# Kernel optimization log

Hardware: AMD Instinct MI355X
Metric: run time of the kernel (lower is better)

## Reference

```python
import jax, jax.numpy as jnp
import numpy as np

LN_EPS = 1e-3  # Keras LayerNormalization default epsilon
EPS = 1e-8     # slot-attention weight epsilon
NUM_ITERS = 3


def layer_norm(x, g, b):
    m = jnp.mean(x, axis=-1, keepdims=True)
    v = jnp.var(x, axis=-1, keepdims=True)
    return g * (x - m) * jax.lax.rsqrt(v + LN_EPS) + b


def gru_cell(x, h, Wx, Wh, b_in, b_rec):
    # Keras GRUCell (reset_after=True): separate input and recurrent biases
    gx = x @ Wx + b_in      # [K, 3D]
    gh = h @ Wh + b_rec     # [K, 3D]
    xz, xr, xh = jnp.split(gx, 3, axis=-1)
    hz, hr, hh = jnp.split(gh, 3, axis=-1)
    z = jax.nn.sigmoid(xz + hz)
    r = jax.nn.sigmoid(xr + hr)
    h_cand = jnp.tanh(xh + r * hh)
    return z * h + (1.0 - z) * h_cand


def setup_inputs() -> dict:
    key = jax.random.key(0)
    N, C, D, H, K = 262144, 64, 64, 128, 4
    ks = jax.random.split(key, 32)
    w = lambda k, s: (jax.random.normal(k, s, jnp.float32) * 0.02)
    inp = {
        "x": jax.random.normal(ks[0], (N, C), jnp.float32),
        "noise_fg": jax.random.normal(ks[1], (K - 1, D), jnp.float32),
        "noise_bg": jax.random.normal(ks[2], (1, D), jnp.float32),
        "ln_in_g": jnp.ones((C,), jnp.float32),
        "ln_in_b": jnp.zeros((C,), jnp.float32),
        "mu_fg": w(ks[3], (1, D)),
        "log_sigma_fg": w(ks[4], (1, D)),
        "mu_bg": w(ks[5], (1, D)),
        "log_sigma_bg": w(ks[6], (1, D)),
        "Wk": w(ks[7], (C, D)),
        "Wv": w(ks[8], (C, D)),
        "qfg_g": jnp.ones((D,), jnp.float32),
        "qfg_b": jnp.zeros((D,), jnp.float32),
        "Wq_fg": w(ks[9], (D, D)),
        "qbg_g": jnp.ones((D,), jnp.float32),
        "qbg_b": jnp.zeros((D,), jnp.float32),
        "Wq_bg": w(ks[10], (D, D)),
        "gru_fg_Wx": w(ks[11], (D, 3 * D)),
        "gru_fg_Wh": w(ks[12], (D, 3 * D)),
        "gru_fg_bin": jnp.zeros((3 * D,), jnp.float32),
        "gru_fg_brec": jnp.zeros((3 * D,), jnp.float32),
        "gru_bg_Wx": w(ks[13], (D, 3 * D)),
        "gru_bg_Wh": w(ks[14], (D, 3 * D)),
        "gru_bg_bin": jnp.zeros((3 * D,), jnp.float32),
        "gru_bg_brec": jnp.zeros((3 * D,), jnp.float32),
        "mfg_g": jnp.ones((D,), jnp.float32),
        "mfg_b": jnp.zeros((D,), jnp.float32),
        "mfg_W1": w(ks[15], (D, H)),
        "mfg_b1": jnp.zeros((H,), jnp.float32),
        "mfg_W2": w(ks[16], (H, D)),
        "mfg_b2": jnp.zeros((D,), jnp.float32),
        "mbg_g": jnp.ones((D,), jnp.float32),
        "mbg_b": jnp.zeros((D,), jnp.float32),
        "mbg_W1": w(ks[17], (D, H)),
        "mbg_b1": jnp.zeros((H,), jnp.float32),
        "mbg_W2": w(ks[18], (H, D)),
        "mbg_b2": jnp.zeros((D,), jnp.float32),
    }
    return inp


def reference(x, noise_fg, noise_bg, ln_in_g, ln_in_b, mu_fg, log_sigma_fg, mu_bg,
              log_sigma_bg, Wk, Wv, qfg_g, qfg_b, Wq_fg, qbg_g, qbg_b, Wq_bg,
              gru_fg_Wx, gru_fg_Wh, gru_fg_bin, gru_fg_brec,
              gru_bg_Wx, gru_bg_Wh, gru_bg_bin, gru_bg_brec,
              mfg_g, mfg_b, mfg_W1, mfg_b1, mfg_W2, mfg_b2,
              mbg_g, mbg_b, mbg_W1, mbg_b1, mbg_W2, mbg_b2):
    D = Wk.shape[1]
    scale = D ** (-0.5)
    x = layer_norm(x, ln_in_g, ln_in_b)
    k = x @ Wk  # [N, D]
    v = x @ Wv  # [N, D]
    slots_fg = mu_fg + jnp.exp(log_sigma_fg) * noise_fg  # [K-1, D]
    slots_bg = mu_bg + jnp.exp(log_sigma_bg) * noise_bg  # [1, D]
    attn = None
    for _ in range(NUM_ITERS):
        q_fg = layer_norm(slots_fg, qfg_g, qfg_b) @ Wq_fg * scale  # [K-1, D]
        q_bg = layer_norm(slots_bg, qbg_g, qbg_b) @ Wq_bg * scale  # [1, D]
        logits = jnp.concatenate([k @ q_bg.T, k @ q_fg.T], axis=-1)  # [N, K]
        attn = jax.nn.softmax(logits, axis=-1)  # competition over slots
        w_all = attn + EPS
        w_all = w_all / jnp.sum(w_all, axis=0, keepdims=True)  # normalize over N
        updates = w_all.T @ v  # [K, D]
        upd_bg, upd_fg = updates[:1], updates[1:]
        slots_bg = gru_cell(upd_bg, slots_bg, gru_bg_Wx, gru_bg_Wh, gru_bg_bin, gru_bg_brec)
        slots_fg = gru_cell(upd_fg, slots_fg, gru_fg_Wx, gru_fg_Wh, gru_fg_bin, gru_fg_brec)
        h_bg = jax.nn.relu(layer_norm(slots_bg, mbg_g, mbg_b) @ mbg_W1 + mbg_b1)
        slots_bg = slots_bg + h_bg @ mbg_W2 + mbg_b2
        h_fg = jax.nn.relu(layer_norm(slots_fg, mfg_g, mfg_b) @ mfg_W1 + mfg_b1)
        slots_fg = slots_fg + h_fg @ mfg_W2 + mfg_b2
    slots = jnp.concatenate([slots_bg, slots_fg], axis=0)  # [K, D]
    return slots, attn.T  # attn: [K, N]
```

## Files before the change

kernel.cpp:

```cpp
#include <hip/hip_runtime.h>
#include <hip/hip_bf16.h>

#define N_ROWS   262144
#define TILES    1024
#define LN_EPS_F 1e-3f
#define EPS_W    1e-8f
#define NEPS_F   (262144.0f*1e-8f)

__device__ __forceinline__ float bf2f(unsigned u){ return __uint_as_float((u&0xffffu)<<16); }
__device__ __forceinline__ ushort f2bf(float f){
  unsigned u = __float_as_uint(f);
  return (ushort)((u + 0x7fffu + ((u>>16)&1u)) >> 16);
}
__device__ __forceinline__ unsigned cvtpk(float lo, float hi){
  unsigned r;
  asm("v_cvt_pk_bf16_f32 %0, %1, %2" : "=v"(r) : "v"(lo), "v"(hi));
  return r;
}
__device__ __forceinline__ float wave_sum64(float v){
#pragma unroll
  for (int off=1; off<64; off<<=1) v += __shfl_xor(v, off);
  return v;
}

__global__ __launch_bounds__(256) void attn_pass_kernel(
    const float* __restrict__ x, uint* __restrict__ xhat,
    const float* __restrict__ ucoef, float* __restrict__ pT,
    float* __restrict__ attn_out, int first, int last)
{
  __shared__ __align__(16) ushort xs[64*256];
  __shared__ __align__(16) uint2 attn_s[256];
  __shared__ __align__(16) float qs[256];
  __shared__ float qc[4];
  const int tid = threadIdx.x;
  const int w = tid>>6, ln = tid&63;
  const int lm = ln&15, lg = ln>>4;
  qs[tid] = ucoef[tid];
  if (tid < 4) qc[tid] = ucoef[256+tid];

  const size_t r0 = (size_t)blockIdx.x*256;

  if (first){
#pragma unroll
    for (int mi = 0; mi < 4; ++mi){
      const int trow = w*64 + mi*16 + lm;
      const float* xr = &x[(r0 + trow)*64 + lg*8];
      const float4 a0 = *(const float4*)xr;
      const float4 a1 = *(const float4*)(xr+4);
      const float4 b0 = *(const float4*)(xr+32);
      const float4 b1 = *(const float4*)(xr+36);
      float s1 = ((a0.x+a0.y)+(a0.z+a0.w)) + ((a1.x+a1.y)+(a1.z+a1.w))
               + ((b0.x+b0.y)+(b0.z+b0.w)) + ((b1.x+b1.y)+(b1.z+b1.w));
      float s2 = a0.x*a0.x; s2=fmaf(a0.y,a0.y,s2); s2=fmaf(a0.z,a0.z,s2); s2=fmaf(a0.w,a0.w,s2);
      s2=fmaf(a1.x,a1.x,s2); s2=fmaf(a1.y,a1.y,s2); s2=fmaf(a1.z,a1.z,s2); s2=fmaf(a1.w,a1.w,s2);
      s2=fmaf(b0.x,b0.x,s2); s2=fmaf(b0.y,b0.y,s2); s2=fmaf(b0.z,b0.z,s2); s2=fmaf(b0.w,b0.w,s2);
      s2=fmaf(b1.x,b1.x,s2); s2=fmaf(b1.y,b1.y,s2); s2=fmaf(b1.z,b1.z,s2); s2=fmaf(b1.w,b1.w,s2);
      s1 += __shfl_xor(s1,16); s2 += __shfl_xor(s2,16);
      s1 += __shfl_xor(s1,32); s2 += __shfl_xor(s2,32);
      const float m  = s1*(1.0f/64.0f);
      const float rs = rsqrtf(s2*(1.0f/64.0f) - m*m + LN_EPS_F);
      const float nm = -m*rs;
      float xv[16];
      xv[0]=fmaf(a0.x,rs,nm); xv[1]=fmaf(a0.y,rs,nm); xv[2]=fmaf(a0.z,rs,nm); xv[3]=fmaf(a0.w,rs,nm);
      xv[4]=fmaf(a1.x,rs,nm); xv[5]=fmaf(a1.y,rs,nm); xv[6]=fmaf(a1.z,rs,nm); xv[7]=fmaf(a1.w,rs,nm);
      xv[8]=fmaf(b0.x,rs,nm); xv[9]=fmaf(b0.y,rs,nm); xv[10]=fmaf(b0.z,rs,nm); xv[11]=fmaf(b0.w,rs,nm);
      xv[12]=fmaf(b1.x,rs,nm); xv[13]=fmaf(b1.y,rs,nm); xv[14]=fmaf(b1.z,rs,nm); xv[15]=fmaf(b1.w,rs,nm);
      const int ch = trow>>3, rr2 = trow&7;
#pragma unroll
      for (int p = 0; p < 8; ++p){
        const int d = lg*8 + p;
        xs[d*256 + ((ch ^ ((d*5)&31))<<3) + rr2] = (ushort)cvtpk(xv[p], xv[p]);
      }
#pragma unroll
      for (int p = 0; p < 8; ++p){
        const int d = 32 + lg*8 + p;
        xs[d*256 + ((ch ^ ((d*5)&31))<<3) + rr2] = (ushort)cvtpk(xv[8+p], xv[8+p]);
      }
    }
    __syncthreads();
#pragma unroll
    for (int k = 0; k < 8; ++k){
      const int i = k*256 + tid;
      const uint4 v = *(const uint4*)&xs[i*8];
      *(uint4*)&xhat[(size_t)blockIdx.x*8192 + i*4] = v;
    }
  } else {
#pragma unroll
    for (int k = 0; k < 8; ++k){
      const int i = k*256 + tid;
      const uint4 v = *(const uint4*)&xhat[(size_t)blockIdx.x*8192 + i*4];
      *(uint4*)&xs[i*8] = v;
    }
    __syncthreads();
  }

  const int lrow = w*64 + lm*4;
  float la[4][4];
#pragma unroll
  for (int r = 0; r < 4; ++r)
#pragma unroll
    for (int s = 0; s < 4; ++s) la[r][s] = 0.f;
#pragma unroll
  for (int dd = 0; dd < 16; ++dd){
    const int d = lg*16 + dd;
    const uint2 kk = *(const uint2*)&xs[d*256 + (((lrow>>3) ^ ((d*5)&31))<<3) + (lrow&7)];
    const float e0 = bf2f(kk.x), e1 = bf2f(kk.x>>16);
    const float e2 = bf2f(kk.y), e3 = bf2f(kk.y>>16);
    const float4 q4 = *(const float4*)&qs[d*4];
#pragma unroll
    for (int s = 0; s < 4; ++s){
      const float qv = (s==0)?q4.x:(s==1)?q4.y:(s==2)?q4.z:q4.w;
      la[0][s] = fmaf(e0, qv, la[0][s]);
      la[1][s] = fmaf(e1, qv, la[1][s]);
      la[2][s] = fmaf(e2, qv, la[2][s]);
      la[3][s] = fmaf(e3, qv, la[3][s]);
    }
  }
#pragma unroll
  for (int r = 0; r < 4; ++r)
#pragma unroll
    for (int s = 0; s < 4; ++s){
      la[r][s] += __shfl_xor(la[r][s], 16);
      la[r][s] += __shfl_xor(la[r][s], 32);
      la[r][s] += qc[s];
    }

  float av[4][4];
  float cs0=0.f, cs1=0.f, cs2=0.f, cs3=0.f;
#pragma unroll
  for (int r = 0; r < 4; ++r){
    const float mx = fmaxf(fmaxf(la[r][0],la[r][1]), fmaxf(la[r][2],la[r][3]));
    const float e0 = __expf(la[r][0]-mx), e1 = __expf(la[r][1]-mx);
    const float e2 = __expf(la[r][2]-mx), e3 = __expf(la[r][3]-mx);
    const float inv = 1.0f/((e0+e1)+(e2+e3));
    av[r][0]=e0*inv; av[r][1]=e1*inv; av[r][2]=e2*inv; av[r][3]=e3*inv;
    cs0 += av[r][0]; cs1 += av[r][1]; cs2 += av[r][2]; cs3 += av[r][3];
  }
  if (lg == 0){
#pragma unroll
    for (int r = 0; r < 4; ++r){
      uint2 pk;
      pk.x = cvtpk(av[r][0], av[r][1]);
      pk.y = cvtpk(av[r][2], av[r][3]);
      attn_s[lrow + r] = pk;
    }
    if (last){
#pragma unroll
      for (int s = 0; s < 4; ++s){
        float4 o; o.x=av[0][s]; o.y=av[1][s]; o.z=av[2][s]; o.w=av[3][s];
        *(float4*)&attn_out[(size_t)s*N_ROWS + r0 + lrow] = o;
      }
    }
  }
  cs0 = wave_sum64(cs0)*0.25f; cs1 = wave_sum64(cs1)*0.25f;
  cs2 = wave_sum64(cs2)*0.25f; cs3 = wave_sum64(cs3)*0.25f;

  float n0=0.f,n1=0.f,n2=0.f,n3=0.f, vs=0.f;
#pragma unroll
  for (int rb = 0; rb < 8; ++rb){
    const int ch = w*8 + rb;
    const uint4 vv = *(const uint4*)&xs[ln*256 + ((ch ^ ((ln*5)&31))<<3)];
    const ushort* vp = (const ushort*)&vv;
#pragma unroll
    for (int k2 = 0; k2 < 8; ++k2){
      const uint2 au = attn_s[ch*8 + k2];
      const float b0 = bf2f(au.x), b1 = bf2f(au.x>>16);
      const float b2 = bf2f(au.y), b3 = bf2f(au.y>>16);
      const float vvv = bf2f((unsigned)vp[k2]);
      n0 = fmaf(b0, vvv, n0); n1 = fmaf(b1, vvv, n1);
      n2 = fmaf(b2, vvv, n2); n3 = fmaf(b3, vvv, n3);
      vs += vvv;
    }
  }

  __syncthreads();
  float* fp = (float*)xs;
  fp[w*256 + 0*64 + ln] = n0;
  fp[w*256 + 1*64 + ln] = n1;
  fp[w*256 + 2*64 + ln] = n2;
  fp[w*256 + 3*64 + ln] = n3;
  fp[1024 + w*64 + ln] = vs;
  if (ln == 0){ fp[1280+w*4+0]=cs0; fp[1280+w*4+1]=cs1; fp[1280+w*4+2]=cs2; fp[1280+w*4+3]=cs3; }
  __syncthreads();
  float* pb = pT + (size_t)blockIdx.x*324;
  pb[tid] = fp[tid] + fp[256+tid] + fp[512+tid] + fp[768+tid];
  if (tid < 64)
    pb[256 + tid] = fp[1024+tid] + fp[1088+tid] + fp[1152+tid] + fp[1216+tid];
  if (tid < 4)
    pb[320 + tid] = fp[1280+tid] + fp[1284+tid] + fp[1288+tid] + fp[1292+tid];
}

__global__ __launch_bounds__(512) void update_kernel(int mode,
    const float* __restrict__ pT,
    float* __restrict__ slots, float* __restrict__ ucoef, float* __restrict__ out,
    const float* __restrict__ noise_fg, const float* __restrict__ noise_bg,
    const float* __restrict__ mu_fg, const float* __restrict__ ls_fg,
    const float* __restrict__ mu_bg, const float* __restrict__ ls_bg,
    const float* __restrict__ ln_g, const float* __restrict__ ln_b,
    const float* __restrict__ Wk, const float* __restrict__ Wv,
    const float* __restrict__ qfg_g, const float* __restrict__ qfg_b, const float* __restrict__ Wq_fg,
    const float* __restrict__ qbg_g, const float* __restrict__ qbg_b, const float* __restrict__ Wq_bg,
    const float* __restrict__ gfWx, const float* __restrict__ gfWh,
    const float* __restrict__ gfbin, const float* __restrict__ gfbrec,
    const float* __restrict__ gbWx, const float* __restrict__ gbWh,
    const float* __restrict__ gbbin, const float* __restrict__ gbbrec,
    const float* __restrict__ mfg_g, const float* __restrict__ mfg_b,
    const float* __restrict__ mfW1, const float* __restrict__ mfb1,
    const float* __restrict__ mfW2, const float* __restrict__ mfb2,
    const float* __restrict__ mbg_g, const float* __restrict__ mbg_b,
    const float* __restrict__ mbW1, const float* __restrict__ mbb1,
    const float* __restrict__ mbW2, const float* __restrict__ mbb2)
{
  const int j = blockIdx.x;
  const int tid = threadIdx.x;
  const int ln = tid & 63, wv = tid >> 6;
  const bool bg = (j == 0);

  __shared__ __align__(16) float wlds[24640];
  __shared__ float bi_s[192], br_s[192], b1_s[128], b2_s[64];
  __shared__ float mg_s[64], mbv_s[64], qg_s[64], qb_s[64], gl_s[64], bl_s[64];
  __shared__ float vin_s[64], u_s[64], h_s[64], hg_s[64], l_s[64], h1_s[128], ql_s[64];
  __shared__ float gxp[2][192], ghp[2][192];
  __shared__ float pn_s[8][64], pv_s[8][64], csw[8];
  __shared__ float p4[4][128], p8[8][64];

  const float* __restrict__ Wx = bg?gbWx:gfWx;  const float* __restrict__ Wh = bg?gbWh:gfWh;
  const float* __restrict__ bi = bg?gbbin:gfbin; const float* __restrict__ br = bg?gbbrec:gfbrec;
  const float* __restrict__ W1 = bg?mbW1:mfW1;  const float* __restrict__ b1 = bg?mbb1:mfb1;
  const float* __restrict__ W2 = bg?mbW2:mfW2;  const float* __restrict__ b2 = bg?mbb2:mfb2;
  const float* __restrict__ Wq = bg?Wq_bg:Wq_fg;

  const int WQOFF  = (mode == 0) ? 0 : 16384;
  const int WKTOFF = (mode == 0) ? 4096 : 20480;

  float hnew = 0.f;

  if (mode == 0) {
    { const float4* s = (const float4*)Wq; float4* d = (float4*)wlds;
#pragma unroll
      for (int i = 0; i < 2; ++i) d[tid + i*512] = s[tid + i*512]; }
#pragma unroll
    for (int k = 0; k < 8; ++k){
      const int i = tid + k*512;
      wlds[4096 + (i&63)*65 + (i>>6)] = Wk[i];
    }
    if (tid < 64){
      qg_s[tid] = (bg?qbg_g:qfg_g)[tid]; qb_s[tid] = (bg?qbg_b:qfg_b)[tid];
      gl_s[tid] = ln_g[tid]; bl_s[tid] = ln_b[tid];
      hnew = bg ? fmaf(expf(ls_bg[tid]), noise_bg[tid], mu_bg[tid])
                : fmaf(expf(ls_fg[tid]), noise_fg[(j-1)*64+tid], mu_fg[tid]);
      slots[j*64 + tid] = hnew;
    }
    __syncthreads();
  } else {
    if (tid < 192){ bi_s[tid] = bi[tid]; br_s[tid] = br[tid]; }
    else if (tid < 320){ const int i2 = tid-192; b1_s[i2] = b1[i2]; }
    else if (tid < 384){ const int i2 = tid-320; b2_s[i2] = b2[i2]; }
    else if (tid < 448){ const int i2 = tid-384; mg_s[i2] = (bg?mbg_g:mfg_g)[i2]; mbv_s[i2] = (bg?mbg_b:mfg_b)[i2]; }
    else               { const int i2 = tid-448; qg_s[i2] = (bg?qbg_g:qfg_g)[i2]; qb_s[i2] = (bg?qbg_b:qfg_b)[i2]; }
    if (tid < 64){ gl_s[tid] = ln_g[tid]; bl_s[tid] = ln_b[tid]; }
    { const float4* sA = (const float4*)Wx; const float4* sB = (const float4*)Wh;
      float4* dA = (float4*)wlds; float4* dB = (float4*)(wlds + 12288);
#pragma unroll
      for (int i = 0; i < 6; ++i){ dA[tid + i*512] = sA[tid + i*512]; dB[tid + i*512] = sB[tid + i*512]; } }

    {
      float a0 = 0.f, a1 = 0.f, a2 = 0.f;
      float c0 = 0.f, c1v = 0.f, c2v = 0.f;
      for (int bb = 0; bb < TILES/8; bb += 16){
#pragma unroll
        for (int u = 0; u < 16; u += 2){
          const float* pa = pT + (size_t)((bb+u  )*8 + wv)*324;
          const float* pc = pT + (size_t)((bb+u+1)*8 + wv)*324;
          a0 += pa[j*64 + ln];  a1 += pa[256 + ln];  a2 += pa[320 + j];
          c0 += pc[j*64 + ln];  c1v += pc[256 + ln]; c2v += pc[320 + j];
        }
      }
      pn_s[wv][ln] = a0 + c0; pv_s[wv][ln] = a1 + c1v;
      if (ln == 0) csw[wv] = a2 + c2v;
    }
    if (tid < 64) h_s[tid] = slots[j*64 + tid];
    __syncthreads();
    if (tid < 64) {
      const float csum = ((csw[0]+csw[1])+(csw[2]+csw[3])) + ((csw[4]+csw[5])+(csw[6]+csw[7])) + NEPS_F;
      float nm = 0.f, vm = 0.f;
#pragma unroll
      for (int p2 = 0; p2 < 8; ++p2){ nm += pn_s[p2][tid]; vm += pv_s[p2][tid]; }
      vin_s[tid] = gl_s[tid]*(nm + EPS_W*vm)/csum + bl_s[tid];
    }
    __syncthreads();
    { const int p8i = tid >> 6;
      float a = 0.f;
      float wbuf[8];
#pragma unroll
      for (int dd = 0; dd < 8; ++dd) wbuf[dd] = Wv[(p8i*8+dd)*64 + ln];
#pragma unroll
      for (int dd = 0; dd < 8; ++dd) a = fmaf(vin_s[p8i*8+dd], wbuf[dd], a);
      p8[p8i][ln] = a;
    }
    __syncthreads();
    if (tid < 64)
      u_s[tid] = ((p8[0][tid]+p8[1][tid])+(p8[2][tid]+p8[3][tid]))
               + ((p8[4][tid]+p8[5][tid])+(p8[6][tid]+p8[7][tid]));
    __syncthreads();
    if (tid < 384) {
      const int gcol = tid % 192, gp = tid / 192;
      float ax = 0.f, ah = 0.f;
#pragma unroll
      for (int dd = 0; dd < 32; ++dd) {
        ax = fmaf(u_s[gp*32+dd], wlds[(gp*32+dd)*192 + gcol], ax);
        ah = fmaf(h_s[gp*32+dd], wlds[12288 + (gp*32+dd)*192 + gcol], ah);
      }
      gxp[gp][gcol] = ax; ghp[gp][gcol] = ah;
    }
    __syncthreads();
    { const float4* s1 = (const float4*)W1; const float4* s2 = (const float4*)W2; const float4* s3 = (const float4*)Wq;
      float4* d1 = (float4*)wlds; float4* d2 = (float4*)(wlds + 8192); float4* d3 = (float4*)(wlds + 16384);
#pragma unroll
      for (int i = 0; i < 4; ++i){ d1[tid + i*512] = s1[tid + i*512]; d2[tid + i*512] = s2[tid + i*512]; }
#pragma unroll
      for (int i = 0; i < 2; ++i){ d3[tid + i*512] = s3[tid + i*512]; }
#pragma unroll
      for (int k = 0; k < 8; ++k){
        const int i = tid + k*512;
        wlds[20480 + (i&63)*65 + (i>>6)] = Wk[i];
      } }
    if (tid < 64) {
      const float gx0 = gxp[0][tid]     + gxp[1][tid]     + bi_s[tid];
      const float gh0 = ghp[0][tid]     + ghp[1][tid]     + br_s[tid];
      const float gx1 = gxp[0][64+tid]  + gxp[1][64+tid]  + bi_s[64+tid];
      const float gh1 = ghp[0][64+tid]  + ghp[1][64+tid]  + br_s[64+tid];
      const float gx2 = gxp[0][128+tid] + gxp[1][128+tid] + bi_s[128+tid];
      const float gh2 = ghp[0][128+tid] + ghp[1][128+tid] + br_s[128+tid];
      const float h  = h_s[tid];
      const float z  = 1.f/(1.f + expf(-(gx0 + gh0)));
      const float rr = 1.f/(1.f + expf(-(gx1 + gh1)));
      const float hc = tanhf(gx2 + rr*gh2);
      const float hg = z*h + (1.f - z)*hc;
      hg_s[tid] = hg;
      const float m  = wave_sum64(hg) * (1.f/64.f);
      const float vr = wave_sum64((hg-m)*(hg-m)) * (1.f/64.f);
      const float rs = rsqrtf(vr + LN_EPS_F);
      l_s[tid] = mg_s[tid]*(hg-m)*rs + mbv_s[tid];
    }
    __syncthreads();
    { const int p4i = tid >> 7, hi = tid & 127;
      float a = 0.f;
#pragma unroll
      for (int dd = 0; dd < 16; ++dd) a = fmaf(l_s[p4i*16+dd], wlds[(p4i*16+dd)*128 + hi], a);
      p4[p4i][hi] = a;
    }
    __syncthreads();
    if (tid < 128) h1_s[tid] = fmaxf(((p4[0][tid]+p4[1][tid])+(p4[2][tid]+p4[3][tid])) + b1_s[tid], 0.f);
    __syncthreads();
    { const int p8i = tid >> 6;
      float a = 0.f;
#pragma unroll
      for (int dd = 0; dd < 16; ++dd) a = fmaf(h1_s[p8i*16+dd], wlds[8192 + (p8i*16+dd)*64 + ln], a);
      p8[p8i][ln] = a;
    }
    __syncthreads();
    if (tid < 64) {
      hnew = hg_s[tid] + b2_s[tid]
           + ((p8[0][tid]+p8[1][tid])+(p8[2][tid]+p8[3][tid]))
           + ((p8[4][tid]+p8[5][tid])+(p8[6][tid]+p8[7][tid]));
      slots[j*64 + tid] = hnew;
    }
  }

  if (mode == 3) {
    if (tid < 64) out[j*64 + tid] = hnew;
  } else {
    if (tid < 64) {
      const float m  = wave_sum64(hnew) * (1.f/64.f);
      const float vr = wave_sum64((hnew-m)*(hnew-m)) * (1.f/64.f);
      const float rs = rsqrtf(vr + LN_EPS_F);
      l_s[tid] = qg_s[tid]*(hnew-m)*rs + qb_s[tid];
    }
    __syncthreads();
    { const int p8i = tid >> 6;
      float a = 0.f;
#pragma unroll
      for (int dd = 0; dd < 8; ++dd) a = fmaf(l_s[p8i*8+dd], wlds[WQOFF + (p8i*8+dd)*64 + ln], a);
      p8[p8i][ln] = a;
    }
    __syncthreads();
    if (tid < 64)
      ql_s[tid] = (((p8[0][tid]+p8[1][tid])+(p8[2][tid]+p8[3][tid]))
                  +((p8[4][tid]+p8[5][tid])+(p8[6][tid]+p8[7][tid]))) * 0.125f;
    __syncthreads();
    if (tid < 256){
      const int d = tid & 63, pt = tid >> 6;
      float ts = 0.f;
#pragma unroll
      for (int oo = 0; oo < 16; ++oo){
        const int o = pt*16 + oo;
        ts = fmaf(wlds[WKTOFF + o*65 + d], ql_s[o], ts);
      }
      p8[pt][d] = ts;
    }
    __syncthreads();
    if (tid < 64){
      const float t = (p8[0][tid]+p8[1][tid]) + (p8[2][tid]+p8[3][tid]);
      ucoef[tid*4 + j] = gl_s[tid]*t;
      const float c = wave_sum64(bl_s[tid]*t);
      if (tid == 0) ucoef[256 + j] = c;
    }
  }
}

extern "C" void kernel_launch(void* const* d_in, const int* in_sizes, int n_in,
                              void* d_out, int out_size, void* d_ws, size_t ws_size,
                              hipStream_t stream)
{
  const float* x        = (const float*)d_in[0];
  const float* noise_fg = (const float*)d_in[1];
  const float* noise_bg = (const float*)d_in[2];
  const float* ln_g     = (const float*)d_in[3];
  const float* ln_b     = (const float*)d_in[4];
  const float* mu_fg    = (const float*)d_in[5];
  const float* ls_fg    = (const float*)d_in[6];
  const float* mu_bg    = (const float*)d_in[7];
  const float* ls_bg    = (const float*)d_in[8];
  const float* Wk       = (const float*)d_in[9];
  const float* Wv       = (const float*)d_in[10];
  const float* qfg_g    = (const float*)d_in[11];
  const float* qfg_b    = (const float*)d_in[12];
  const float* Wq_fg    = (const float*)d_in[13];
  const float* qbg_g    = (const float*)d_in[14];
  const float* qbg_b    = (const float*)d_in[15];
  const float* Wq_bg    = (const float*)d_in[16];
  const float* gfWx     = (const float*)d_in[17];
  const float* gfWh     = (const float*)d_in[18];
  const float* gfbin    = (const float*)d_in[19];
  const float* gfbrec   = (const float*)d_in[20];
  const float* gbWx     = (const float*)d_in[21];
  const float* gbWh     = (const float*)d_in[22];
  const float* gbbin    = (const float*)d_in[23];
  const float* gbbrec   = (const float*)d_in[24];
  const float* mfg_g    = (const float*)d_in[25];
  const float* mfg_b    = (const float*)d_in[26];
  const float* mfW1     = (const float*)d_in[27];
  const float* mfb1     = (const float*)d_in[28];
  const float* mfW2     = (const float*)d_in[29];
  const float* mfb2     = (const float*)d_in[30];
  const float* mbg_g    = (const float*)d_in[31];
  const float* mbg_b    = (const float*)d_in[32];
  const float* mbW1     = (const float*)d_in[33];
  const float* mbb1     = (const float*)d_in[34];
  const float* mbW2     = (const float*)d_in[35];
  const float* mbb2     = (const float*)d_in[36];

  float* out = (float*)d_out;

  char* ws = (char*)d_ws;
  uint*  xhat  = (uint*)ws;
  float* fws   = (float*)(ws + (size_t)TILES*8192*4);
  float* slots = fws;
  float* ucoef = fws + 256;
  float* pT    = fws + 1024;

  auto launch_update = [&](int mode){
    update_kernel<<<4, 512, 0, stream>>>(mode, pT, slots, ucoef, out,
      noise_fg, noise_bg, mu_fg, ls_fg, mu_bg, ls_bg, ln_g, ln_b, Wk, Wv,
      qfg_g, qfg_b, Wq_fg, qbg_g, qbg_b, Wq_bg,
      gfWx, gfWh, gfbin, gfbrec, gbWx, gbWh, gbbin, gbbrec,
      mfg_g, mfg_b, mfW1, mfb1, mfW2, mfb2,
      mbg_g, mbg_b, mbW1, mbb1, mbW2, mbb2);
  };

  launch_update(0);
  for (int it = 0; it < 3; ++it) {
    attn_pass_kernel<<<TILES, 256, 0, stream>>>(x, xhat, ucoef, pT, out + 256,
                                                it==0 ? 1 : 0, it==2 ? 1 : 0);
    launch_update(it+1);
  }
}
```

Baseline: 109.7 us.

## Fuse initial slot/query setup into first attention pass and process two tiles per block

Removes the separate mode-0 update launch by having every attention block recompute the initial slots, layer norm, query projection and Wk folding itself, with block 0 writing the slots. The attention kernel now runs 512 blocks that each handle two 256-row chunks, accumulating partials across chunks and prefetching the next chunk's xhat into registers while the current one computes. This halves the partial-sum count the update kernel must reduce and drops one launch. In exchange, every block redoes small redundant matmuls in the first pass and there are fewer blocks to spread across CUs.

```diff
diff --git a/kernel.cpp b/kernel.cpp
--- a/kernel.cpp
+++ b/kernel.cpp
@@ -2,16 +2,13 @@
 #include <hip/hip_bf16.h>
 
 #define N_ROWS   262144
-#define TILES    1024
+#define ATT_BLOCKS 512
+#define CHUNKS   2
 #define LN_EPS_F 1e-3f
 #define EPS_W    1e-8f
 #define NEPS_F   (262144.0f*1e-8f)
 
 __device__ __forceinline__ float bf2f(unsigned u){ return __uint_as_float((u&0xffffu)<<16); }
-__device__ __forceinline__ ushort f2bf(float f){
-  unsigned u = __float_as_uint(f);
-  return (ushort)((u + 0x7fffu + ((u>>16)&1u)) >> 16);
-}
 __device__ __forceinline__ unsigned cvtpk(float lo, float hi){
   unsigned r;
   asm("v_cvt_pk_bf16_f32 %0, %1, %2" : "=v"(r) : "v"(lo), "v"(hi));
@@ -26,154 +23,209 @@
 __global__ __launch_bounds__(256) void attn_pass_kernel(
     const float* __restrict__ x, uint* __restrict__ xhat,
     const float* __restrict__ ucoef, float* __restrict__ pT,
-    float* __restrict__ attn_out, int first, int last)
+    float* __restrict__ attn_out, float* __restrict__ slots,
+    const float* __restrict__ noise_fg, const float* __restrict__ noise_bg,
+    const float* __restrict__ mu_fg, const float* __restrict__ ls_fg,
+    const float* __restrict__ mu_bg, const float* __restrict__ ls_bg,
+    const float* __restrict__ ln_g, const float* __restrict__ ln_b,
+    const float* __restrict__ Wk,
+    const float* __restrict__ qfg_g, const float* __restrict__ qfg_b, const float* __restrict__ Wq_fg,
+    const float* __restrict__ qbg_g, const float* __restrict__ qbg_b, const float* __restrict__ Wq_bg,
+    int first, int last)
 {
   __shared__ __align__(16) ushort xs[64*256];
   __shared__ __align__(16) uint2 attn_s[256];
   __shared__ __align__(16) float qs[256];
   __shared__ float qc[4];
+  __shared__ float l4[256], q4s[256];
   const int tid = threadIdx.x;
   const int w = tid>>6, ln = tid&63;
   const int lm = ln&15, lg = ln>>4;
-  qs[tid] = ucoef[tid];
-  if (tid < 4) qc[tid] = ucoef[256+tid];
-
-  const size_t r0 = (size_t)blockIdx.x*256;
+  const int blk = blockIdx.x;
 
   if (first){
-#pragma unroll
-    for (int mi = 0; mi < 4; ++mi){
-      const int trow = w*64 + mi*16 + lm;
-      const float* xr = &x[(r0 + trow)*64 + lg*8];
-      const float4 a0 = *(const float4*)xr;
-      const float4 a1 = *(const float4*)(xr+4);
-      const float4 b0 = *(const float4*)(xr+32);
-      const float4 b1 = *(const float4*)(xr+36);
-      float s1 = ((a0.x+a0.y)+(a0.z+a0.w)) + ((a1.x+a1.y)+(a1.z+a1.w))
-               + ((b0.x+b0.y)+(b0.z+b0.w)) + ((b1.x+b1.y)+(b1.z+b1.w));
-      float s2 = a0.x*a0.x; s2=fmaf(a0.y,a0.y,s2); s2=fmaf(a0.z,a0.z,s2); s2=fmaf(a0.w,a0.w,s2);
-      s2=fmaf(a1.x,a1.x,s2); s2=fmaf(a1.y,a1.y,s2); s2=fmaf(a1.z,a1.z,s2); s2=fmaf(a1.w,a1.w,s2);
-      s2=fmaf(b0.x,b0.x,s2); s2=fmaf(b0.y,b0.y,s2); s2=fmaf(b0.z,b0.z,s2); s2=fmaf(b0.w,b0.w,s2);
-      s2=fmaf(b1.x,b1.x,s2); s2=fmaf(b1.y,b1.y,s2); s2=fmaf(b1.z,b1.z,s2); s2=fmaf(b1.w,b1.w,s2);
-      s1 += __shfl_xor(s1,16); s2 += __shfl_xor(s2,16);
-      s1 += __shfl_xor(s1,32); s2 += __shfl_xor(s2,32);
-      const float m  = s1*(1.0f/64.0f);
-      const float rs = rsqrtf(s2*(1.0f/64.0f) - m*m + LN_EPS_F);
-      const float nm = -m*rs;
-      float xv[16];
-      xv[0]=fmaf(a0.x,rs,nm); xv[1]=fmaf(a0.y,rs,nm); xv[2]=fmaf(a0.z,rs,nm); xv[3]=fmaf(a0.w,rs,nm);
-      xv[4]=fmaf(a1.x,rs,nm); xv[5]=fmaf(a1.y,rs,nm); xv[6]=fmaf(a1.z,rs,nm); xv[7]=fmaf(a1.w,rs,nm);
-      xv[8]=fmaf(b0.x,rs,nm); xv[9]=fmaf(b0.y,rs,nm); xv[10]=fmaf(b0.z,rs,nm); xv[11]=fmaf(b0.w,rs,nm);
-      xv[12]=fmaf(b1.x,rs,nm); xv[13]=fmaf(b1.y,rs,nm); xv[14]=fmaf(b1.z,rs,nm); xv[15]=fmaf(b1.w,rs,nm);
-      const int ch = trow>>3, rr2 = trow&7;
-#pragma unroll
-      for (int p = 0; p < 8; ++p){
-        const int d = lg*8 + p;
-        xs[d*256 + ((ch ^ ((d*5)&31))<<3) + rr2] = (ushort)cvtpk(xv[p], xv[p]);
-      }
-#pragma unroll
-      for (int p = 0; p < 8; ++p){
-        const int d = 32 + lg*8 + p;
-        xs[d*256 + ((ch ^ ((d*5)&31))<<3) + rr2] = (ushort)cvtpk(xv[8+p], xv[8+p]);
-      }
-    }
+    const float h0 = (w==0) ? fmaf(expf(ls_bg[ln]), noise_bg[ln], mu_bg[ln])
+                            : fmaf(expf(ls_fg[ln]), noise_fg[(w-1)*64+ln], mu_fg[ln]);
+    if (blk == 0) slots[w*64+ln] = h0;
+    const float m  = wave_sum64(h0) * (1.f/64.f);
+    const float vr = wave_sum64((h0-m)*(h0-m)) * (1.f/64.f);
+    const float rs = rsqrtf(vr + LN_EPS_F);
+    l4[tid] = (w==0?qbg_g:qfg_g)[ln]*(h0-m)*rs + (w==0?qbg_b:qfg_b)[ln];
     __syncthreads();
-#pragma unroll
-    for (int k = 0; k < 8; ++k){
-      const int i = k*256 + tid;
-      const uint4 v = *(const uint4*)&xs[i*8];
-      *(uint4*)&xhat[(size_t)blockIdx.x*8192 + i*4] = v;
+    {
+      const float* __restrict__ Wqj = (w==0) ? Wq_bg : Wq_fg;
+      float acc = 0.f;
+#pragma unroll
+      for (int dd = 0; dd < 64; ++dd) acc = fmaf(l4[w*64+dd], Wqj[dd*64+ln], acc);
+      q4s[tid] = acc * 0.125f;
+    }
+    __syncthreads();
+    {
+      float t = 0.f;
+#pragma unroll
+      for (int oo = 0; oo < 64; ++oo) t = fmaf(Wk[ln*64+oo], q4s[w*64+oo], t);
+      qs[ln*4 + w] = ln_g[ln]*t;
+      const float cc = wave_sum64(ln_b[ln]*t);
+      if (ln == 0) qc[w] = cc;
     }
   } else {
-#pragma unroll
-    for (int k = 0; k < 8; ++k){
-      const int i = k*256 + tid;
-      const uint4 v = *(const uint4*)&xhat[(size_t)blockIdx.x*8192 + i*4];
-      *(uint4*)&xs[i*8] = v;
-    }
-    __syncthreads();
-  }
-
-  const int lrow = w*64 + lm*4;
-  float la[4][4];
-#pragma unroll
-  for (int r = 0; r < 4; ++r)
-#pragma unroll
-    for (int s = 0; s < 4; ++s) la[r][s] = 0.f;
-#pragma unroll
-  for (int dd = 0; dd < 16; ++dd){
-    const int d = lg*16 + dd;
-    const uint2 kk = *(const uint2*)&xs[d*256 + (((lrow>>3) ^ ((d*5)&31))<<3) + (lrow&7)];
-    const float e0 = bf2f(kk.x), e1 = bf2f(kk.x>>16);
-    const float e2 = bf2f(kk.y), e3 = bf2f(kk.y>>16);
-    const float4 q4 = *(const float4*)&qs[d*4];
-#pragma unroll
-    for (int s = 0; s < 4; ++s){
-      const float qv = (s==0)?q4.x:(s==1)?q4.y:(s==2)?q4.z:q4.w;
-      la[0][s] = fmaf(e0, qv, la[0][s]);
-      la[1][s] = fmaf(e1, qv, la[1][s]);
-      la[2][s] = fmaf(e2, qv, la[2][s]);
-      la[3][s] = fmaf(e3, qv, la[3][s]);
-    }
-  }
-#pragma unroll
-  for (int r = 0; r < 4; ++r)
-#pragma unroll
-    for (int s = 0; s < 4; ++s){
-      la[r][s] += __shfl_xor(la[r][s], 16);
-      la[r][s] += __shfl_xor(la[r][s], 32);
-      la[r][s] += qc[s];
-    }
-
-  float av[4][4];
+    qs[tid] = ucoef[tid];
+    if (tid < 4) qc[tid] = ucoef[256+tid];
+  }
+  __syncthreads();
+
+  float n0=0.f,n1=0.f,n2=0.f,n3=0.f, vs=0.f;
   float cs0=0.f, cs1=0.f, cs2=0.f, cs3=0.f;
-#pragma unroll
-  for (int r = 0; r < 4; ++r){
-    const float mx = fmaxf(fmaxf(la[r][0],la[r][1]), fmaxf(la[r][2],la[r][3]));
-    const float e0 = __expf(la[r][0]-mx), e1 = __expf(la[r][1]-mx);
-    const float e2 = __expf(la[r][2]-mx), e3 = __expf(la[r][3]-mx);
-    const float inv = 1.0f/((e0+e1)+(e2+e3));
-    av[r][0]=e0*inv; av[r][1]=e1*inv; av[r][2]=e2*inv; av[r][3]=e3*inv;
-    cs0 += av[r][0]; cs1 += av[r][1]; cs2 += av[r][2]; cs3 += av[r][3];
-  }
-  if (lg == 0){
+
+  auto compute_chunk = [&](int c){
+    const size_t rg = (size_t)blk*(CHUNKS*256) + (size_t)c*256;
+    const int lrow = w*64 + lm*4;
+    float la[4][4] = {};
+#pragma unroll
+    for (int dd = 0; dd < 16; ++dd){
+      const int d = lg*16 + dd;
+      const uint2 kk = *(const uint2*)&xs[d*256 + (((lrow>>3) ^ ((d*5)&31))<<3) + (lrow&7)];
+      const float e0 = bf2f(kk.x), e1 = bf2f(kk.x>>16);
+      const float e2 = bf2f(kk.y), e3 = bf2f(kk.y>>16);
+      const float4 q4 = *(const float4*)&qs[d*4];
+#pragma unroll
+      for (int s = 0; s < 4; ++s){
+        const float qv = (s==0)?q4.x:(s==1)?q4.y:(s==2)?q4.z:q4.w;
+        la[0][s] = fmaf(e0, qv, la[0][s]);
+        la[1][s] = fmaf(e1, qv, la[1][s]);
+        la[2][s] = fmaf(e2, qv, la[2][s]);
+        la[3][s] = fmaf(e3, qv, la[3][s]);
+      }
+    }
+#pragma unroll
+    for (int r = 0; r < 4; ++r)
+#pragma unroll
+      for (int s = 0; s < 4; ++s){
+        la[r][s] += __shfl_xor(la[r][s], 16);
+        la[r][s] += __shfl_xor(la[r][s], 32);
+        la[r][s] += qc[s];
+      }
+    float av[4][4];
 #pragma unroll
     for (int r = 0; r < 4; ++r){
-      uint2 pk;
-      pk.x = cvtpk(av[r][0], av[r][1]);
-      pk.y = cvtpk(av[r][2], av[r][3]);
-      attn_s[lrow + r] = pk;
-    }
-    if (last){
-#pragma unroll
-      for (int s = 0; s < 4; ++s){
-        float4 o; o.x=av[0][s]; o.y=av[1][s]; o.z=av[2][s]; o.w=av[3][s];
-        *(float4*)&attn_out[(size_t)s*N_ROWS + r0 + lrow] = o;
-      }
-    }
-  }
+      const float mx = fmaxf(fmaxf(la[r][0],la[r][1]), fmaxf(la[r][2],la[r][3]));
+      const float e0 = __expf(la[r][0]-mx), e1 = __expf(la[r][1]-mx);
+      const float e2 = __expf(la[r][2]-mx), e3 = __expf(la[r][3]-mx);
+      const float inv = 1.0f/((e0+e1)+(e2+e3));
+      av[r][0]=e0*inv; av[r][1]=e1*inv; av[r][2]=e2*inv; av[r][3]=e3*inv;
+      cs0 += av[r][0]; cs1 += av[r][1]; cs2 += av[r][2]; cs3 += av[r][3];
+    }
+    if (lg == 0){
+#pragma unroll
+      for (int r = 0; r < 4; ++r){
+        uint2 pk;
+        pk.x = cvtpk(av[r][0], av[r][1]);
+        pk.y = cvtpk(av[r][2], av[r][3]);
+        attn_s[lrow + r] = pk;
+      }
+      if (last){
+#pragma unroll
+        for (int s = 0; s < 4; ++s){
+          float4 o; o.x=av[0][s]; o.y=av[1][s]; o.z=av[2][s]; o.w=av[3][s];
+          *(float4*)&attn_out[(size_t)s*N_ROWS + rg + lrow] = o;
+        }
+      }
+    }
+#pragma unroll
+    for (int rb = 0; rb < 8; ++rb){
+      const int ch = w*8 + rb;
+      const uint4 vv = *(const uint4*)&xs[ln*256 + ((ch ^ ((ln*5)&31))<<3)];
+      const ushort* vp = (const ushort*)&vv;
+#pragma unroll
+      for (int k2 = 0; k2 < 8; ++k2){
+        const uint2 au = attn_s[ch*8 + k2];
+        const float b0 = bf2f(au.x), b1 = bf2f(au.x>>16);
+        const float b2 = bf2f(au.y), b3 = bf2f(au.y>>16);
+        const float vvv = bf2f((unsigned)vp[k2]);
+        n0 = fmaf(b0, vvv, n0); n1 = fmaf(b1, vvv, n1);
+        n2 = fmaf(b2, vvv, n2); n3 = fmaf(b3, vvv, n3);
+        vs += vvv;
+      }
+    }
+  };
+
+  if (first){
+    for (int c = 0; c < CHUNKS; ++c){
+      const size_t rg = (size_t)blk*(CHUNKS*256) + (size_t)c*256;
+#pragma unroll
+      for (int mi = 0; mi < 4; ++mi){
+        const int trow = w*64 + mi*16 + lm;
+        const float* xr = &x[(rg + trow)*64 + lg*8];
+        const float4 a0 = *(const float4*)xr;
+        const float4 a1 = *(const float4*)(xr+4);
+        const float4 b0 = *(const float4*)(xr+32);
+        const float4 b1 = *(const float4*)(xr+36);
+        float s1 = ((a0.x+a0.y)+(a0.z+a0.w)) + ((a1.x+a1.y)+(a1.z+a1.w))
+                 + ((b0.x+b0.y)+(b0.z+b0.w)) + ((b1.x+b1.y)+(b1.z+b1.w));
+        float s2 = a0.x*a0.x; s2=fmaf(a0.y,a0.y,s2); s2=fmaf(a0.z,a0.z,s2); s2=fmaf(a0.w,a0.w,s2);
+        s2=fmaf(a1.x,a1.x,s2); s2=fmaf(a1.y,a1.y,s2); s2=fmaf(a1.z,a1.z,s2); s2=fmaf(a1.w,a1.w,s2);
+        s2=fmaf(b0.x,b0.x,s2); s2=fmaf(b0.y,b0.y,s2); s2=fmaf(b0.z,b0.z,s2); s2=fmaf(b0.w,b0.w,s2);
+        s2=fmaf(b1.x,b1.x,s2); s2=fmaf(b1.y,b1.y,s2); s2=fmaf(b1.z,b1.z,s2); s2=fmaf(b1.w,b1.w,s2);
+        s1 += __shfl_xor(s1,16); s2 += __shfl_xor(s2,16);
+        s1 += __shfl_xor(s1,32); s2 += __shfl_xor(s2,32);
+        const float m  = s1*(1.0f/64.0f);
+        const float rs = rsqrtf(s2*(1.0f/64.0f) - m*m + LN_EPS_F);
+        const float nm = -m*rs;
+        float xv[16];
+        xv[0]=fmaf(a0.x,rs,nm); xv[1]=fmaf(a0.y,rs,nm); xv[2]=fmaf(a0.z,rs,nm); xv[3]=fmaf(a0.w,rs,nm);
+        xv[4]=fmaf(a1.x,rs,nm); xv[5]=fmaf(a1.y,rs,nm); xv[6]=fmaf(a1.z,rs,nm); xv[7]=fmaf(a1.w,rs,nm);
+        xv[8]=fmaf(b0.x,rs,nm); xv[9]=fmaf(b0.y,rs,nm); xv[10]=fmaf(b0.z,rs,nm); xv[11]=fmaf(b0.w,rs,nm);
+        xv[12]=fmaf(b1.x,rs,nm); xv[13]=fmaf(b1.y,rs,nm); xv[14]=fmaf(b1.z,rs,nm); xv[15]=fmaf(b1.w,rs,nm);
+        const int ch = trow>>3, rr2 = trow&7;
+#pragma unroll
+        for (int p = 0; p < 8; ++p){
+          const int d = lg*8 + p;
+          xs[d*256 + ((ch ^ ((d*5)&31))<<3) + rr2] = (ushort)cvtpk(xv[p], xv[p]);
+        }
+#pragma unroll
+        for (int p = 0; p < 8; ++p){
+          const int d = 32 + lg*8 + p;
+          xs[d*256 + ((ch ^ ((d*5)&31))<<3) + rr2] = (ushort)cvtpk(xv[8+p], xv[8+p]);
+        }
+      }
+      __syncthreads();
+      const size_t tile = (size_t)(blk*CHUNKS + c);
+#pragma unroll
+      for (int k = 0; k < 8; ++k){
+        const int i = k*256 + tid;
+        *(uint4*)&xhat[tile*8192 + i*4] = *(const uint4*)&xs[i*8];
+      }
+      compute_chunk(c);
+      __syncthreads();
+    }
+  } else {
+    uint4 sv[8];
+    {
+      const size_t t0 = (size_t)blk*CHUNKS;
+#pragma unroll
+      for (int k = 0; k < 8; ++k){ const int i = k*256 + tid; sv[k] = *(const uint4*)&xhat[t0*8192 + i*4]; }
+#pragma unroll
+      for (int k = 0; k < 8; ++k){ const int i = k*256 + tid; *(uint4*)&xs[i*8] = sv[k]; }
+      __syncthreads();
+    }
+    for (int c = 0; c < CHUNKS; ++c){
+      if (c+1 < CHUNKS){
+        const size_t tl = (size_t)(blk*CHUNKS + c + 1);
+#pragma unroll
+        for (int k = 0; k < 8; ++k){ const int i = k*256 + tid; sv[k] = *(const uint4*)&xhat[tl*8192 + i*4]; }
+      }
+      compute_chunk(c);
+      __syncthreads();
+      if (c+1 < CHUNKS){
+#pragma unroll
+        for (int k = 0; k < 8; ++k){ const int i = k*256 + tid; *(uint4*)&xs[i*8] = sv[k]; }
+        __syncthreads();
+      }
+    }
+  }
+
   cs0 = wave_sum64(cs0)*0.25f; cs1 = wave_sum64(cs1)*0.25f;
   cs2 = wave_sum64(cs2)*0.25f; cs3 = wave_sum64(cs3)*0.25f;
-
-  float n0=0.f,n1=0.f,n2=0.f,n3=0.f, vs=0.f;
-#pragma unroll
-  for (int rb = 0; rb < 8; ++rb){
-    const int ch = w*8 + rb;
-    const uint4 vv = *(const uint4*)&xs[ln*256 + ((ch ^ ((ln*5)&31))<<3)];
-    const ushort* vp = (const ushort*)&vv;
-#pragma unroll
-    for (int k2 = 0; k2 < 8; ++k2){
-      const uint2 au = attn_s[ch*8 + k2];
-      const float b0 = bf2f(au.x), b1 = bf2f(au.x>>16);
-      const float b2 = bf2f(au.y), b3 = bf2f(au.y>>16);
-      const float vvv = bf2f((unsigned)vp[k2]);
-      n0 = fmaf(b0, vvv, n0); n1 = fmaf(b1, vvv, n1);
-      n2 = fmaf(b2, vvv, n2); n3 = fmaf(b3, vvv, n3);
-      vs += vvv;
-    }
-  }
-
-  __syncthreads();
   float* fp = (float*)xs;
   fp[w*256 + 0*64 + ln] = n0;
   fp[w*256 + 1*64 + ln] = n1;
@@ -182,7 +234,7 @@
   fp[1024 + w*64 + ln] = vs;
   if (ln == 0){ fp[1280+w*4+0]=cs0; fp[1280+w*4+1]=cs1; fp[1280+w*4+2]=cs2; fp[1280+w*4+3]=cs3; }
   __syncthreads();
-  float* pb = pT + (size_t)blockIdx.x*324;
+  float* pb = pT + (size_t)blk*324;
   pb[tid] = fp[tid] + fp[256+tid] + fp[512+tid] + fp[768+tid];
   if (tid < 64)
     pb[256 + tid] = fp[1024+tid] + fp[1088+tid] + fp[1152+tid] + fp[1216+tid];
@@ -193,9 +245,6 @@
 __global__ __launch_bounds__(512) void update_kernel(int mode,
     const float* __restrict__ pT,
     float* __restrict__ slots, float* __restrict__ ucoef, float* __restrict__ out,
-    const float* __restrict__ noise_fg, const float* __restrict__ noise_bg,
-    const float* __restrict__ mu_fg, const float* __restrict__ ls_fg,
-    const float* __restrict__ mu_bg, const float* __restrict__ ls_bg,
     const float* __restrict__ ln_g, const float* __restrict__ ln_b,
     const float* __restrict__ Wk, const float* __restrict__ Wv,
     const float* __restrict__ qfg_g, const float* __restrict__ qfg_b, const float* __restrict__ Wq_fg,
@@ -230,142 +279,120 @@
   const float* __restrict__ W2 = bg?mbW2:mfW2;  const float* __restrict__ b2 = bg?mbb2:mfb2;
   const float* __restrict__ Wq = bg?Wq_bg:Wq_fg;
 
-  const int WQOFF  = (mode == 0) ? 0 : 16384;
-  const int WKTOFF = (mode == 0) ? 4096 : 20480;
-
   float hnew = 0.f;
 
-  if (mode == 0) {
-    { const float4* s = (const float4*)Wq; float4* d = (float4*)wlds;
-#pragma unroll
-      for (int i = 0; i < 2; ++i) d[tid + i*512] = s[tid + i*512]; }
+  if (tid < 192){ bi_s[tid] = bi[tid]; br_s[tid] = br[tid]; }
+  else if (tid < 320){ const int i2 = tid-192; b1_s[i2] = b1[i2]; }
+  else if (tid < 384){ const int i2 = tid-320; b2_s[i2] = b2[i2]; }
+  else if (tid < 448){ const int i2 = tid-384; mg_s[i2] = (bg?mbg_g:mfg_g)[i2]; mbv_s[i2] = (bg?mbg_b:mfg_b)[i2]; }
+  else               { const int i2 = tid-448; qg_s[i2] = (bg?qbg_g:qfg_g)[i2]; qb_s[i2] = (bg?qbg_b:qfg_b)[i2]; }
+  if (tid < 64){ gl_s[tid] = ln_g[tid]; bl_s[tid] = ln_b[tid]; }
+  { const float4* sA = (const float4*)Wx; const float4* sB = (const float4*)Wh;
+    float4* dA = (float4*)wlds; float4* dB = (float4*)(wlds + 12288);
+#pragma unroll
+    for (int i = 0; i < 6; ++i){ dA[tid + i*512] = sA[tid + i*512]; dB[tid + i*512] = sB[tid + i*512]; } }
+
+  {
+    float a0 = 0.f, a1 = 0.f, a2 = 0.f;
+    float c0 = 0.f, c1v = 0.f, c2v = 0.f;
+    for (int bb = 0; bb < ATT_BLOCKS/8; bb += 16){
+#pragma unroll
+      for (int u = 0; u < 16; u += 2){
+        const float* pa = pT + (size_t)((bb+u  )*8 + wv)*324;
+        const float* pc = pT + (size_t)((bb+u+1)*8 + wv)*324;
+        a0 += pa[j*64 + ln];  a1 += pa[256 + ln];  a2 += pa[320 + j];
+        c0 += pc[j*64 + ln];  c1v += pc[256 + ln]; c2v += pc[320 + j];
+      }
+    }
+    pn_s[wv][ln] = a0 + c0; pv_s[wv][ln] = a1 + c1v;
+    if (ln == 0) csw[wv] = a2 + c2v;
+  }
+  if (tid < 64) h_s[tid] = slots[j*64 + tid];
+  __syncthreads();
+  if (tid < 64) {
+    const float csum = ((csw[0]+csw[1])+(csw[2]+csw[3])) + ((csw[4]+csw[5])+(csw[6]+csw[7])) + NEPS_F;
+    float nm = 0.f, vm = 0.f;
+#pragma unroll
+    for (int p2 = 0; p2 < 8; ++p2){ nm += pn_s[p2][tid]; vm += pv_s[p2][tid]; }
+    vin_s[tid] = gl_s[tid]*(nm + EPS_W*vm)/csum + bl_s[tid];
+  }
+  __syncthreads();
+  { const int p8i = tid >> 6;
+    float a = 0.f;
+    float wbuf[8];
+#pragma unroll
+    for (int dd = 0; dd < 8; ++dd) wbuf[dd] = Wv[(p8i*8+dd)*64 + ln];
+#pragma unroll
+    for (int dd = 0; dd < 8; ++dd) a = fmaf(vin_s[p8i*8+dd], wbuf[dd], a);
+    p8[p8i][ln] = a;
+  }
+  __syncthreads();
+  if (tid < 64)
+    u_s[tid] = ((p8[0][tid]+p8[1][tid])+(p8[2][tid]+p8[3][tid]))
+             + ((p8[4][tid]+p8[5][tid])+(p8[6][tid]+p8[7][tid]));
+  __syncthreads();
+  if (tid < 384) {
+    const int gcol = tid % 192, gp = tid / 192;
+    float ax = 0.f, ah = 0.f;
+#pragma unroll
+    for (int dd = 0; dd < 32; ++dd) {
+      ax = fmaf(u_s[gp*32+dd], wlds[(gp*32+dd)*192 + gcol], ax);
+      ah = fmaf(h_s[gp*32+dd], wlds[12288 + (gp*32+dd)*192 + gcol], ah);
+    }
+    gxp[gp][gcol] = ax; ghp[gp][gcol] = ah;
+  }
+  __syncthreads();
+  { const float4* s1 = (const float4*)W1; const float4* s2 = (const float4*)W2; const float4* s3 = (const float4*)Wq;
+    float4* d1 = (float4*)wlds; float4* d2 = (float4*)(wlds + 8192); float4* d3 = (float4*)(wlds + 16384);
+#pragma unroll
+    for (int i = 0; i < 4; ++i){ d1[tid + i*512] = s1[tid + i*512]; d2[tid + i*512] = s2[tid + i*512]; }
+#pragma unroll
+    for (int i = 0; i < 2; ++i){ d3[tid + i*512] = s3[tid + i*512]; }
 #pragma unroll
     for (int k = 0; k < 8; ++k){
       const int i = tid + k*512;
-      wlds[4096 + (i&63)*65 + (i>>6)] = Wk[i];
-    }
-    if (tid < 64){
-      qg_s[tid] = (bg?qbg_g:qfg_g)[tid]; qb_s[tid] = (bg?qbg_b:qfg_b)[tid];
-      gl_s[tid] = ln_g[tid]; bl_s[tid] = ln_b[tid];
-      hnew = bg ? fmaf(expf(ls_bg[tid]), noise_bg[tid], mu_bg[tid])
-                : fmaf(expf(ls_fg[tid]), noise_fg[(j-1)*64+tid], mu_fg[tid]);
-      slots[j*64 + tid] = hnew;
-    }
-    __syncthreads();
-  } else {
-    if (tid < 192){ bi_s[tid] = bi[tid]; br_s[tid] = br[tid]; }
-    else if (tid < 320){ const int i2 = tid-192; b1_s[i2] = b1[i2]; }
-    else if (tid < 384){ const int i2 = tid-320; b2_s[i2] = b2[i2]; }
-    else if (tid < 448){ const int i2 = tid-384; mg_s[i2] = (bg?mbg_g:mfg_g)[i2]; mbv_s[i2] = (bg?mbg_b:mfg_b)[i2]; }
-    else               { const int i2 = tid-448; qg_s[i2] = (bg?qbg_g:qfg_g)[i2]; qb_s[i2] = (bg?qbg_b:qfg_b)[i2]; }
-    if (tid < 64){ gl_s[tid] = ln_g[tid]; bl_s[tid] = ln_b[tid]; }
-    { const float4* sA = (const float4*)Wx; const float4* sB = (const float4*)Wh;
-      float4* dA = (float4*)wlds; float4* dB = (float4*)(wlds + 12288);
-#pragma unroll
-      for (int i = 0; i < 6; ++i){ dA[tid + i*512] = sA[tid + i*512]; dB[tid + i*512] = sB[tid + i*512]; } }
-
-    {
-      float a0 = 0.f, a1 = 0.f, a2 = 0.f;
-      float c0 = 0.f, c1v = 0.f, c2v = 0.f;
-      for (int bb = 0; bb < TILES/8; bb += 16){
-#pragma unroll
-        for (int u = 0; u < 16; u += 2){
-          const float* pa = pT + (size_t)((bb+u  )*8 + wv)*324;
-          const float* pc = pT + (size_t)((bb+u+1)*8 + wv)*324;
-          a0 += pa[j*64 + ln];  a1 += pa[256 + ln];  a2 += pa[320 + j];
-          c0 += pc[j*64 + ln];  c1v += pc[256 + ln]; c2v += pc[320 + j];
-        }
-      }
-      pn_s[wv][ln] = a0 + c0; pv_s[wv][ln] = a1 + c1v;
-      if (ln == 0) csw[wv] = a2 + c2v;
-    }
-    if (tid < 64) h_s[tid] = slots[j*64 + tid];
-    __syncthreads();
-    if (tid < 64) {
-      const float csum = ((csw[0]+csw[1])+(csw[2]+csw[3])) + ((csw[4]+csw[5])+(csw[6]+csw[7])) + NEPS_F;
-      float nm = 0.f, vm = 0.f;
-#pragma unroll
-      for (int p2 = 0; p2 < 8; ++p2){ nm += pn_s[p2][tid]; vm += pv_s[p2][tid]; }
-      vin_s[tid] = gl_s[tid]*(nm + EPS_W*vm)/csum + bl_s[tid];
-    }
-    __syncthreads();
-    { const int p8i = tid >> 6;
-      float a = 0.f;
-      float wbuf[8];
-#pragma unroll
-      for (int dd = 0; dd < 8; ++dd) wbuf[dd] = Wv[(p8i*8+dd)*64 + ln];
-#pragma unroll
-      for (int dd = 0; dd < 8; ++dd) a = fmaf(vin_s[p8i*8+dd], wbuf[dd], a);
-      p8[p8i][ln] = a;
-    }
-    __syncthreads();
-    if (tid < 64)
-      u_s[tid] = ((p8[0][tid]+p8[1][tid])+(p8[2][tid]+p8[3][tid]))
-               + ((p8[4][tid]+p8[5][tid])+(p8[6][tid]+p8[7][tid]));
-    __syncthreads();
-    if (tid < 384) {
-      const int gcol = tid % 192, gp = tid / 192;
-      float ax = 0.f, ah = 0.f;
-#pragma unroll
-      for (int dd = 0; dd < 32; ++dd) {
-        ax = fmaf(u_s[gp*32+dd], wlds[(gp*32+dd)*192 + gcol], ax);
-        ah = fmaf(h_s[gp*32+dd], wlds[12288 + (gp*32+dd)*192 + gcol], ah);
-      }
-      gxp[gp][gcol] = ax; ghp[gp][gcol] = ah;
-    }
-    __syncthreads();
-    { const float4* s1 = (const float4*)W1; const float4* s2 = (const float4*)W2; const float4* s3 = (const float4*)Wq;
-      float4* d1 = (float4*)wlds; float4* d2 = (float4*)(wlds + 8192); float4* d3 = (float4*)(wlds + 16384);
-#pragma unroll
-      for (int i = 0; i < 4; ++i){ d1[tid + i*512] = s1[tid + i*512]; d2[tid + i*512] = s2[tid + i*512]; }
-#pragma unroll
-      for (int i = 0; i < 2; ++i){ d3[tid + i*512] = s3[tid + i*512]; }
-#pragma unroll
-      for (int k = 0; k < 8; ++k){
-        const int i = tid + k*512;
-        wlds[20480 + (i&63)*65 + (i>>6)] = Wk[i];
-      } }
-    if (tid < 64) {
-      const float gx0 = gxp[0][tid]     + gxp[1][tid]     + bi_s[tid];
-      const float gh0 = ghp[0][tid]     + ghp[1][tid]     + br_s[tid];
-      const float gx1 = gxp[0][64+tid]  + gxp[1][64+tid]  + bi_s[64+tid];
-      const float gh1 = ghp[0][64+tid]  + ghp[1][64+tid]  + br_s[64+tid];
-      const float gx2 = gxp[0][128+tid] + gxp[1][128+tid] + bi_s[128+tid];
-      const float gh2 = ghp[0][128+tid] + ghp[1][128+tid] + br_s[128+tid];
-      const float h  = h_s[tid];
-      const float z  = 1.f/(1.f + expf(-(gx0 + gh0)));
-      const float rr = 1.f/(1.f + expf(-(gx1 + gh1)));
-      const float hc = tanhf(gx2 + rr*gh2);
-      const float hg = z*h + (1.f - z)*hc;
-      hg_s[tid] = hg;
-      const float m  = wave_sum64(hg) * (1.f/64.f);
-      const float vr = wave_sum64((hg-m)*(hg-m)) * (1.f/64.f);
-      const float rs = rsqrtf(vr + LN_EPS_F);
-      l_s[tid] = mg_s[tid]*(hg-m)*rs + mbv_s[tid];
-    }
-    __syncthreads();
-    { const int p4i = tid >> 7, hi = tid & 127;
-      float a = 0.f;
-#pragma unroll
-      for (int dd = 0; dd < 16; ++dd) a = fmaf(l_s[p4i*16+dd], wlds[(p4i*16+dd)*128 + hi], a);
-      p4[p4i][hi] = a;
-    }
-    __syncthreads();
-    if (tid < 128) h1_s[tid] = fmaxf(((p4[0][tid]+p4[1][tid])+(p4[2][tid]+p4[3][tid])) + b1_s[tid], 0.f);
-    __syncthreads();
-    { const int p8i = tid >> 6;
-      float a = 0.f;
-#pragma unroll
-      for (int dd = 0; dd < 16; ++dd) a = fmaf(h1_s[p8i*16+dd], wlds[8192 + (p8i*16+dd)*64 + ln], a);
-      p8[p8i][ln] = a;
-    }
-    __syncthreads();
-    if (tid < 64) {
-      hnew = hg_s[tid] + b2_s[tid]
-           + ((p8[0][tid]+p8[1][tid])+(p8[2][tid]+p8[3][tid]))
-           + ((p8[4][tid]+p8[5][tid])+(p8[6][tid]+p8[7][tid]));
-      slots[j*64 + tid] = hnew;
-    }
+      wlds[20480 + (i&63)*65 + (i>>6)] = Wk[i];
+    } }
+  if (tid < 64) {
+    const float gx0 = gxp[0][tid]     + gxp[1][tid]     + bi_s[tid];
+    const float gh0 = ghp[0][tid]     + ghp[1][tid]     + br_s[tid];
+    const float gx1 = gxp[0][64+tid]  + gxp[1][64+tid]  + bi_s[64+tid];
+    const float gh1 = ghp[0][64+tid]  + ghp[1][64+tid]  + br_s[64+tid];
+    const float gx2 = gxp[0][128+tid] + gxp[1][128+tid] + bi_s[128+tid];
+    const float gh2 = ghp[0][128+tid] + ghp[1][128+tid] + br_s[128+tid];
+    const float h  = h_s[tid];
+    const float z  = 1.f/(1.f + expf(-(gx0 + gh0)));
+    const float rr = 1.f/(1.f + expf(-(gx1 + gh1)));
+    const float hc = tanhf(gx2 + rr*gh2);
+    const float hg = z*h + (1.f - z)*hc;
+    hg_s[tid] = hg;
+    const float m  = wave_sum64(hg) * (1.f/64.f);
+    const float vr = wave_sum64((hg-m)*(hg-m)) * (1.f/64.f);
+    const float rs = rsqrtf(vr + LN_EPS_F);
+    l_s[tid] = mg_s[tid]*(hg-m)*rs + mbv_s[tid];
+  }
+  __syncthreads();
+  { const int p4i = tid >> 7, hi = tid & 127;
+    float a = 0.f;
+#pragma unroll
+    for (int dd = 0; dd < 16; ++dd) a = fmaf(l_s[p4i*16+dd], wlds[(p4i*16+dd)*128 + hi], a);
+    p4[p4i][hi] = a;
+  }
+  __syncthreads();
+  if (tid < 128) h1_s[tid] = fmaxf(((p4[0][tid]+p4[1][tid])+(p4[2][tid]+p4[3][tid])) + b1_s[tid], 0.f);
+  __syncthreads();
+  { const int p8i = tid >> 6;
+    float a = 0.f;
+#pragma unroll
+    for (int dd = 0; dd < 16; ++dd) a = fmaf(h1_s[p8i*16+dd], wlds[8192 + (p8i*16+dd)*64 + ln], a);
+    p8[p8i][ln] = a;
+  }
+  __syncthreads();
+  if (tid < 64) {
+    hnew = hg_s[tid] + b2_s[tid]
+         + ((p8[0][tid]+p8[1][tid])+(p8[2][tid]+p8[3][tid]))
+         + ((p8[4][tid]+p8[5][tid])+(p8[6][tid]+p8[7][tid]));
+    slots[j*64 + tid] = hnew;
   }
 
   if (mode == 3) {
@@ -381,7 +408,7 @@
     { const int p8i = tid >> 6;
       float a = 0.f;
 #pragma unroll
-      for (int dd = 0; dd < 8; ++dd) a = fmaf(l_s[p8i*8+dd], wlds[WQOFF + (p8i*8+dd)*64 + ln], a);
+      for (int dd = 0; dd < 8; ++dd) a = fmaf(l_s[p8i*8+dd], wlds[16384 + (p8i*8+dd)*64 + ln], a);
       p8[p8i][ln] = a;
     }
     __syncthreads();
@@ -395,7 +422,7 @@
 #pragma unroll
       for (int oo = 0; oo < 16; ++oo){
         const int o = pt*16 + oo;
-        ts = fmaf(wlds[WKTOFF + o*65 + d], ql_s[o], ts);
+        ts = fmaf(wlds[20480 + o*65 + d], ql_s[o], ts);
       }
       p8[pt][d] = ts;
     }
@@ -455,24 +482,30 @@
 
   char* ws = (char*)d_ws;
   uint*  xhat  = (uint*)ws;
-  float* fws   = (float*)(ws + (size_t)TILES*8192*4);
+  float* fws   = (float*)(ws + (size_t)ATT_BLOCKS*CHUNKS*8192*4);
   float* slots = fws;
   float* ucoef = fws + 256;
   float* pT    = fws + 1024;
-
+  float* attn_out = out + 256;
+
+  auto launch_attn = [&](int first, int last){
+    attn_pass_kernel<<<ATT_BLOCKS, 256, 0, stream>>>(x, xhat, ucoef, pT, attn_out, slots,
+      noise_fg, noise_bg, mu_fg, ls_fg, mu_bg, ls_bg, ln_g, ln_b, Wk,
+      qfg_g, qfg_b, Wq_fg, qbg_g, qbg_b, Wq_bg, first, last);
+  };
   auto launch_update = [&](int mode){
     update_kernel<<<4, 512, 0, stream>>>(mode, pT, slots, ucoef, out,
-      noise_fg, noise_bg, mu_fg, ls_fg, mu_bg, ls_bg, ln_g, ln_b, Wk, Wv,
+      ln_g, ln_b, Wk, Wv,
       qfg_g, qfg_b, Wq_fg, qbg_g, qbg_b, Wq_bg,
       gfWx, gfWh, gfbin, gfbrec, gbWx, gbWh, gbbin, gbbrec,
       mfg_g, mfg_b, mfW1, mfb1, mfW2, mfb2,
       mbg_g, mbg_b, mbW1, mbb1, mbW2, mbb2);
   };
 
-  launch_update(0);
-  for (int it = 0; it < 3; ++it) {
-    attn_pass_kernel<<<TILES, 256, 0, stream>>>(x, xhat, ucoef, pT, out + 256,
-                                                it==0 ? 1 : 0, it==2 ? 1 : 0);
-    launch_update(it+1);
-  }
+  launch_attn(1, 0);
+  launch_update(1);
+  launch_attn(0, 0);
+  launch_update(2);
+  launch_attn(0, 1);
+  launch_update(3);
 }
```

Result: no change. 109.4 us, median of 2 (-0.2%).
